# Performance work log

Measured on AMD Instinct MI355X. Metric: run time of the kernel, lower is better.

## Reference

```python
import jax, jax.numpy as jnp
import numpy as np

# Physical / solver constants (mirroring MMSolver class attrs and submodules)
GAMMA_LL = 1.7595e11   # gyromagnetic ratio (MMSolver.gamma_LL)
DT = 5e-12             # timestep [s]
ALPHA_RUN = 0.01       # Damping(relax=False)
ALPHA_RELAX = 0.5      # Damping(relax=True): high damping to relax m
A_EXCH = 3.5e-12       # exchange stiffness [J/m]
DX = 50e-9             # cell size geom.d
MU0 = 4e-7 * np.pi
C_SOT = 1e-4           # SOT strength [T]
RELAX_STEPS = 100      # MMSolver.relax_timesteps
NX, NY = 256, 256
T_STEPS = 256
N_SRC, N_PROBE, N_SIG = 3, 5, 2


def setup_inputs() -> dict:
    key = jax.random.key(0)
    list_signal = jax.random.normal(key, (N_SIG, T_STEPS, N_SRC), jnp.float32) * 1e-3
    # geometry(): constant bias field 60 mT along +y (m0 direction)
    B_ext = jnp.zeros((1, 3, NX, NY), jnp.float32).at[:, 1].set(0.06)
    Msat = jnp.float32(8e5)  # geom.Ms [A/m]
    src_pos = jnp.array([[20, 64], [20, 128], [20, 192]], jnp.int32)
    probe_pos = jnp.array([[230, 42], [230, 85], [230, 128], [230, 170], [230, 213]], jnp.int32)
    return {"list_signal": list_signal, "B_ext": B_ext, "Msat": Msat,
            "src_pos": src_pos, "probe_pos": probe_pos, "final_board": 0}


def _laplacian(m):
    # 5-point stencil with replicate (Neumann) boundaries; m: [1,3,nx,ny]
    mp = jnp.pad(m, ((0, 0), (0, 0), (1, 1), (1, 1)), mode='edge')
    return (mp[:, :, 2:, 1:-1] + mp[:, :, :-2, 1:-1]
            + mp[:, :, 1:-1, 2:] + mp[:, :, 1:-1, :-2] - 4.0 * m)


def _B_eff(m, B_ext, Msat):
    # B_ext + Exchange(m, Msat) + Demag(m, Msat)
    exch = (2.0 * A_EXCH / (Msat * DX * DX)) * _laplacian(m)
    n_demag = jnp.array([0.0, 0.0, 1.0], m.dtype).reshape(1, 3, 1, 1)  # thin-film demag
    demag = -MU0 * Msat * m * n_demag
    return B_ext + exch + demag


def _torque_LLG(m, B_ext, Msat, alpha):
    m_x_Beff = jnp.cross(m, _B_eff(m, B_ext, Msat), axis=1)
    p = jnp.broadcast_to(jnp.array([0.0, 1.0, 0.0], m.dtype).reshape(1, 3, 1, 1), m.shape)
    sot = C_SOT * jnp.cross(m, jnp.cross(m, p, axis=1), axis=1)  # torque_SOT
    return -(1.0 / (1.0 + alpha * alpha)) * (m_x_Beff + alpha * jnp.cross(m, m_x_Beff, axis=1)) + sot


def _rk4_step(m, B_ext, Msat, alpha):
    h = GAMMA_LL * DT
    k1 = _torque_LLG(m, B_ext, Msat, alpha)
    k2 = _torque_LLG(m + 0.5 * h * k1, B_ext, Msat, alpha)
    k3 = _torque_LLG(m + 0.5 * h * k2, B_ext, Msat, alpha)
    k4 = _torque_LLG(m + h * k3, B_ext, Msat, alpha)
    return m + (h / 6.0) * (k1 + 2.0 * k2 + 2.0 * k3 + k4)


def reference(list_signal, B_ext, Msat, src_pos, probe_pos, final_board):
    m0 = jnp.zeros((1, 3, NX, NY), list_signal.dtype).at[:, 1].set(1.0)

    # relax(): 100 high-damping RK4 steps under torch.no_grad()
    Bs = jax.lax.stop_gradient(B_ext)
    Ms = jax.lax.stop_gradient(Msat)
    m_relaxed, _ = jax.lax.scan(lambda m, _: (_rk4_step(m, Bs, Ms, ALPHA_RELAX), None),
                                m0, None, length=RELAX_STEPS)
    m_relaxed = jax.lax.stop_gradient(m_relaxed)

    def step(m, sig_t):
        # inject_sources: add per-source signal to B_z at source cells
        Bx = B_ext.at[0, 2, src_pos[:, 0], src_pos[:, 1]].add(sig_t)
        m_new = _rk4_step(m, Bx, Msat, ALPHA_RUN)
        # measure_probes: z-component at probe cells
        if final_board:
            meas = ((m_new - m_relaxed) * Msat)[0, 2, probe_pos[:, 0], probe_pos[:, 1]]
        else:
            meas = m_new[0, 2, probe_pos[:, 0], probe_pos[:, 1]]
        return m_new, meas

    step_ckpt = jax.checkpoint(step)  # mirrors torch.utils.checkpoint per-step
    outs = []
    for s in range(list_signal.shape[0]):  # forward()'s loop over signals
        _, probes = jax.lax.scan(step_ckpt, m_relaxed, list_signal[s])
        outs.append(probes)  # [T, n_probes]
    return jnp.stack(outs)  # [n_signals, T, n_probes]
```

## Files before the change

kernel.cpp:

```cpp
#include <hip/hip_runtime.h>

constexpr int NX = 256, NY = 256;
constexpr int T_STEPS = 256, N_SRC = 3, N_PROBE = 5;
constexpr int RELAX_STEPS = 100;
constexpr int TILE = 16, HALO = 8, LDIM = 32, LPAIR = 17;
constexpr int NBX = NX / TILE, NBY = NY / TILE;
constexpr int BPS = NBX * NBY;
constexpr int NSIG = 2;
constexpr int NBLOCKS = BPS * NSIG;
constexpr int NTHR = 512;
constexpr int NPAIR = T_STEPS / 2;
constexpr int FIELD = 3 * NX * NY;
constexpr int F_TOTAL = NSIG * 2 * FIELD;
constexpr int FLAG_STRIDE = 16;

constexpr float H_STEP = (float)(175950000000.0 * 5e-12);
constexpr float H_HALF = (float)(175950000000.0 * 5e-12 * 0.5);
constexpr float H_6    = (float)(175950000000.0 * 5e-12 / 6.0);
constexpr float CSOT   = 1e-4f;

typedef float f2 __attribute__((ext_vector_type(2)));
union F2U { f2 v; unsigned long long u; };

__global__ void init_flags(int* flags) {
    flags[blockIdx.x * blockDim.x + threadIdx.x] = 0;
}

__device__ __forceinline__ void torque2(f2 mx, f2 my, f2 mz,
                                        f2 B0, f2 B1, f2 B2,
                                        float pref, float alpha,
                                        f2& o0, f2& o1, f2& o2) {
    const f2 c10 = my * B2 - mz * B1;
    const f2 c11 = mz * B0 - mx * B2;
    const f2 c12 = mx * B1 - my * B0;
    const f2 c20 = my * c12 - mz * c11;
    const f2 c21 = mz * c10 - mx * c12;
    const f2 c22 = mx * c11 - my * c10;
    o0 = pref * (c10 + alpha * c20) + CSOT * (my * mx);
    o1 = pref * (c11 + alpha * c21) - CSOT * (mx * mx + mz * mz);
    o2 = pref * (c12 + alpha * c22) + CSOT * (my * mz);
}

__device__ __forceinline__ void relax_ode2(f2 Bx, f2 By, f2 Bz, float dmg,
                                           f2& r0, f2& r1, f2& r2) {
    r0 = 0.0f; r1 = 1.0f; r2 = 0.0f;
    const float aR = 0.5f;
    const float pR = (float)(-(1.0 / (1.0 + 0.5 * 0.5)));
    for (int it = 0; it < RELAX_STEPS; ++it) {
        f2 k10,k11,k12,k20,k21,k22,k30,k31,k32,k40,k41,k42;
        torque2(r0,r1,r2, Bx,By,Bz - dmg*r2, pR,aR, k10,k11,k12);
        f2 u0=r0+H_HALF*k10, u1=r1+H_HALF*k11, u2=r2+H_HALF*k12;
        torque2(u0,u1,u2, Bx,By,Bz - dmg*u2, pR,aR, k20,k21,k22);
        u0=r0+H_HALF*k20; u1=r1+H_HALF*k21; u2=r2+H_HALF*k22;
        torque2(u0,u1,u2, Bx,By,Bz - dmg*u2, pR,aR, k30,k31,k32);
        u0=r0+H_STEP*k30; u1=r1+H_STEP*k31; u2=r2+H_STEP*k32;
        torque2(u0,u1,u2, Bx,By,Bz - dmg*u2, pR,aR, k40,k41,k42);
        r0 += H_6 * (((k10 + 2.0f*k20) + 2.0f*k30) + k40);
        r1 += H_6 * (((k11 + 2.0f*k21) + 2.0f*k31) + k41);
        r2 += H_6 * (((k12 + 2.0f*k22) + 2.0f*k32) + k42);
    }
}

__device__ __forceinline__ float cohLoad(const float* p) {
    return __hip_atomic_load(p, __ATOMIC_RELAXED, __HIP_MEMORY_SCOPE_AGENT);
}
__device__ __forceinline__ f2 cohLoad2(const float* p) {
    F2U x; x.u = __hip_atomic_load((const unsigned long long*)p,
                                   __ATOMIC_RELAXED, __HIP_MEMORY_SCOPE_AGENT);
    return x.v;
}
__device__ __forceinline__ void cohStore2(float* p, f2 v) {
    F2U x; x.v = v;
    __hip_atomic_store((unsigned long long*)p, x.u,
                       __ATOMIC_RELAXED, __HIP_MEMORY_SCOPE_AGENT);
}

__global__ __launch_bounds__(NTHR, 4)
void mm_kernel(const float* __restrict__ sig,
               const float* __restrict__ Bext,
               const float* __restrict__ MsatP,
               const int*   __restrict__ srcp,
               const int*   __restrict__ prbp,
               const int*   __restrict__ fbP,
               float* __restrict__ out,
               float* __restrict__ F,
               int*   __restrict__ flags)
{
    __shared__ f2 bufA[3][LDIM][LPAIR];
    __shared__ f2 bufB[3][LDIM][LPAIR];

    const int tid = threadIdx.x;
    const int blk = blockIdx.x;
    const int sg = blk & 1;
    const int b  = blk >> 1;
    const int tbx = b / NBY, tby = b % NBY;
    const int x0 = tbx * TILE, y0 = tby * TILE;
    const bool atT = (tbx == 0), atB = (tbx == NBX - 1);
    const bool atL = (tby == 0), atR = (tby == NBY - 1);

    const float Msat = MsatP[0];
    const float cex = 7e-12f / (Msat * 5e-8f * 5e-8f);
    const float dmg = (float)(4e-7 * 3.14159265358979323846) * Msat;
    const int fb = fbP[0];
    const float alpha = 0.01f;
    const float pref  = (float)(-(1.0 / (1.0 + 0.01 * 0.01)));

    const int r  = tid >> 4;
    const int pp = tid & 15;
    const int c2 = pp << 1;
    const int gx  = x0 - HALO + r;
    const int gy0 = y0 - HALO + c2;
    const int gy1 = gy0 + 1;
    const int gxc  = min(max(gx, 0), NX - 1);
    const int gyc0 = min(max(gy0, 0), NY - 1);
    const int gyc1 = min(max(gy1, 0), NY - 1);
    const bool cUp = (gxc == 0), cDn = (gxc == NX - 1);
    const bool cL  = (gyc0 == 0), cR  = (gyc1 == NY - 1);
    const bool interior = (r >= HALO && r < HALO + TILE &&
                           c2 >= HALO && c2 < HALO + TILE);
    const bool pairOK = (gy0 >= 0 && gy0 <= NY - 2);
    const int srcFlagIdx = sg * BPS + (gxc >> 4) * NBY + (gyc0 >> 4);

    int sid0 = -1, sid1 = -1, pid0 = -1, pid1 = -1;
    for (int k = 0; k < N_SRC; ++k) {
        if (srcp[2*k] == gxc && srcp[2*k+1] == gyc0) sid0 = k;
        if (srcp[2*k] == gxc && srcp[2*k+1] == gyc1) sid1 = k;
    }
    if (interior)
        for (int k = 0; k < N_PROBE; ++k) {
            if (prbp[2*k] == gx && prbp[2*k+1] == gy0) pid0 = k;
            if (prbp[2*k] == gx && prbp[2*k+1] == gy1) pid1 = k;
        }

    const f2 bX = { Bext[0*NX*NY + gxc*NY + gyc0], Bext[0*NX*NY + gxc*NY + gyc1] };
    const f2 bY = { Bext[1*NX*NY + gxc*NY + gyc0], Bext[1*NX*NY + gxc*NY + gyc1] };
    const f2 bZ = { Bext[2*NX*NY + gxc*NY + gyc0], Bext[2*NX*NY + gxc*NY + gyc1] };

    f2 m0, m1, m2;
    relax_ode2(bX, bY, bZ, dmg, m0, m1, m2);
    const f2 mrelz = m2;

    f2 a0 = 0.f, a1 = 0.f, a2 = 0.f;
    f2 f0, f1, f2v;

    float* Fsig = F + (size_t)sg * 2 * FIELD;
    int* myflag = flags + (sg * BPS + b) * FLAG_STRIDE;

    bufA[0][r][pp] = m0; bufA[1][r][pp] = m1; bufA[2][r][pp] = m2;
    f0 = m0; f1 = m1; f2v = m2;

    for (int pr = 0; pr < NPAIR; ++pr) {
        if (pr > 0 && !interior) {
            const int* fp = flags + srcFlagIdx * FLAG_STRIDE;
            while (__hip_atomic_load(fp, __ATOMIC_RELAXED,
                                     __HIP_MEMORY_SCOPE_AGENT) < pr)
                __builtin_amdgcn_s_sleep(1);
            const float* Fin = Fsig + (size_t)(pr & 1) * FIELD;
            if (pairOK) {
                const int g0 = gxc * NY + gy0;
                m0 = cohLoad2(Fin + g0);
                m1 = cohLoad2(Fin + NX*NY + g0);
                m2 = cohLoad2(Fin + 2*NX*NY + g0);
            } else {
                const int gg = gxc * NY + gyc0;
                const float v0 = cohLoad(Fin + gg);
                const float v1 = cohLoad(Fin + NX*NY + gg);
                const float v2 = cohLoad(Fin + 2*NX*NY + gg);
                m0 = f2{v0, v0}; m1 = f2{v1, v1}; m2 = f2{v2, v2};
            }
            bufA[0][r][pp] = m0; bufA[1][r][pp] = m1; bufA[2][r][pp] = m2;
            f0 = m0; f1 = m1; f2v = m2;
        }
        f2 b2cs[2] = { bZ, bZ };
        if (sid0 >= 0) {
            b2cs[0].x = bZ.x + sig[((size_t)sg*T_STEPS + 2*pr    )*N_SRC + sid0];
            b2cs[1].x = bZ.x + sig[((size_t)sg*T_STEPS + 2*pr + 1)*N_SRC + sid0];
        }
        if (sid1 >= 0) {
            b2cs[0].y = bZ.y + sig[((size_t)sg*T_STEPS + 2*pr    )*N_SRC + sid1];
            b2cs[1].y = bZ.y + sig[((size_t)sg*T_STEPS + 2*pr + 1)*N_SRC + sid1];
        }
        __syncthreads();

        for (int p = 0; p < 2; ++p) {
            const f2 b2c = b2cs[p];

            for (int s = 1; s <= 4; ++s) {
                const int sh = 4*p + s;
                const int loi = atT ? HALO : sh;
                const int hiI = atB ? HALO + TILE - 1 : LDIM - 1 - sh;
                const int loj = atL ? HALO : sh;
                const int hiJ = atR ? HALO + TILE - 1 : LDIM - 1 - sh;
                const float cc = (s <= 2) ? H_HALF : H_STEP;
                const float w  = (s == 1 || s == 4) ? 1.0f : 2.0f;
                const f2 (*P)[LDIM][LPAIR] = (sh & 1) ? bufA : bufB;
                f2 (*Q)[LDIM][LPAIR] = (sh & 1) ? bufB : bufA;

                const bool active = (r >= loi && r <= hiI &&
                                     c2 + 1 >= loj && c2 <= hiJ);
                if (active) {
                    const f2 fo[3] = { f0, f1, f2v };
                    f2 l[3];
                    #pragma unroll
                    for (int ch = 0; ch < 3; ++ch) {
                        const f2 up = cUp ? fo[ch] : P[ch][r-1][pp];
                        const f2 dn = cDn ? fo[ch] : P[ch][r+1][pp];
                        const float lfs = __shfl_up(fo[ch].y, 1);
                        const float rts = __shfl_down(fo[ch].x, 1);
                        const float lf = cL ? fo[ch].x : lfs;
                        const float rt = cR ? fo[ch].y : rts;
                        const f2 rgt = { fo[ch].y, rt };
                        const f2 lft = { lf, fo[ch].x };
                        l[ch] = dn + up + rgt + lft - 4.f * fo[ch];
                    }
                    f2 t0, t1, t2;
                    torque2(f0, f1, f2v,
                            bX + cex * l[0],
                            bY + cex * l[1],
                            b2c + cex * l[2] - dmg * f2v,
                            pref, alpha, t0, t1, t2);
                    if (s < 4) {
                        const bool inr = (r >= (atT ? HALO : 4*p + 4) &&
                                          r <= (atB ? HALO+TILE-1 : 27 - 4*p) &&
                                          c2 >= (atL ? HALO : 4*p + 4) &&
                                          c2 <= (atR ? HALO+TILE-1 : 27 - 4*p));
                        if (inr) { a0 += w*t0; a1 += w*t1; a2 += w*t2; }
                        f0 = m0 + cc*t0; f1 = m1 + cc*t1; f2v = m2 + cc*t2;
                        Q[0][r][pp] = f0; Q[1][r][pp] = f1; Q[2][r][pp] = f2v;
                    } else {
                        a0 += w*t0; a1 += w*t1; a2 += w*t2;
                        m0 += H_6*a0; m1 += H_6*a1; m2 += H_6*a2;
                        a0 = 0.f; a1 = 0.f; a2 = 0.f;
                        f0 = m0; f1 = m1; f2v = m2;
                        Q[0][r][pp] = m0; Q[1][r][pp] = m1; Q[2][r][pp] = m2;
                        const int tt = 2*pr + p;
                        if (pid0 >= 0)
                            out[((size_t)sg*T_STEPS + tt)*N_PROBE + pid0] =
                                fb ? (m2.x - mrelz.x)*Msat : m2.x;
                        if (pid1 >= 0)
                            out[((size_t)sg*T_STEPS + tt)*N_PROBE + pid1] =
                                fb ? (m2.y - mrelz.y)*Msat : m2.y;
                        if (p == 1 && pr + 1 < NPAIR && interior) {
                            float* Fout = Fsig + (size_t)((pr + 1) & 1) * FIELD;
                            const int g0 = gx * NY + gy0;
                            cohStore2(Fout + g0,          m0);
                            cohStore2(Fout + NX*NY + g0,  m1);
                            cohStore2(Fout + 2*NX*NY + g0, m2);
                        }
                    }
                }
                if (p == 1 && s == 4 && pr + 1 < NPAIR)
                    __builtin_amdgcn_s_waitcnt(0);
                __syncthreads();
            }
        }
        if (pr + 1 < NPAIR && tid == 0)
            __hip_atomic_store(myflag, pr + 1, __ATOMIC_RELAXED,
                               __HIP_MEMORY_SCOPE_AGENT);
    }
}

extern "C" void kernel_launch(void* const* d_in, const int* in_sizes, int n_in,
                              void* d_out, int out_size, void* d_ws, size_t ws_size,
                              hipStream_t stream) {
    const float* sigp = (const float*)d_in[0];
    const float* Bext = (const float*)d_in[1];
    const float* Msat = (const float*)d_in[2];
    const int*   srcp = (const int*)d_in[3];
    const int*   prbp = (const int*)d_in[4];
    const int*   fbP  = (const int*)d_in[5];
    float* outp = (float*)d_out;
    float* F    = (float*)d_ws;
    int*   flags = (int*)((char*)d_ws + (size_t)F_TOTAL * sizeof(float));

    init_flags<<<NBLOCKS * FLAG_STRIDE / 256, 256, 0, stream>>>(flags);

    void* args[] = { (void*)&sigp, (void*)&Bext, (void*)&Msat, (void*)&srcp,
                     (void*)&prbp, (void*)&fbP, (void*)&outp, (void*)&F,
                     (void*)&flags };
    hipLaunchCooperativeKernel((void*)mm_kernel, dim3(NBLOCKS), dim3(NTHR),
                               args, 0, stream);
}
```

Measured before the change: 1.169 ms.

## Process both signals in one block with float4 lanes instead of separate blocks

```diff
diff --git a/kernel.cpp b/kernel.cpp
--- a/kernel.cpp
+++ b/kernel.cpp
@@ -7,7 +7,7 @@
 constexpr int NBX = NX / TILE, NBY = NY / TILE;
 constexpr int BPS = NBX * NBY;
 constexpr int NSIG = 2;
-constexpr int NBLOCKS = BPS * NSIG;
+constexpr int NBLOCKS = BPS;
 constexpr int NTHR = 512;
 constexpr int NPAIR = T_STEPS / 2;
 constexpr int FIELD = 3 * NX * NY;
@@ -20,41 +20,42 @@
 constexpr float CSOT   = 1e-4f;
 
 typedef float f2 __attribute__((ext_vector_type(2)));
+typedef float f4 __attribute__((ext_vector_type(4)));
 union F2U { f2 v; unsigned long long u; };
 
 __global__ void init_flags(int* flags) {
     flags[blockIdx.x * blockDim.x + threadIdx.x] = 0;
 }
 
-__device__ __forceinline__ void torque2(f2 mx, f2 my, f2 mz,
-                                        f2 B0, f2 B1, f2 B2,
+__device__ __forceinline__ void torque4(f4 mx, f4 my, f4 mz,
+                                        f4 B0, f4 B1, f4 B2,
                                         float pref, float alpha,
-                                        f2& o0, f2& o1, f2& o2) {
-    const f2 c10 = my * B2 - mz * B1;
-    const f2 c11 = mz * B0 - mx * B2;
-    const f2 c12 = mx * B1 - my * B0;
-    const f2 c20 = my * c12 - mz * c11;
-    const f2 c21 = mz * c10 - mx * c12;
-    const f2 c22 = mx * c11 - my * c10;
+                                        f4& o0, f4& o1, f4& o2) {
+    const f4 c10 = my * B2 - mz * B1;
+    const f4 c11 = mz * B0 - mx * B2;
+    const f4 c12 = mx * B1 - my * B0;
+    const f4 c20 = my * c12 - mz * c11;
+    const f4 c21 = mz * c10 - mx * c12;
+    const f4 c22 = mx * c11 - my * c10;
     o0 = pref * (c10 + alpha * c20) + CSOT * (my * mx);
     o1 = pref * (c11 + alpha * c21) - CSOT * (mx * mx + mz * mz);
     o2 = pref * (c12 + alpha * c22) + CSOT * (my * mz);
 }
 
-__device__ __forceinline__ void relax_ode2(f2 Bx, f2 By, f2 Bz, float dmg,
-                                           f2& r0, f2& r1, f2& r2) {
+__device__ __forceinline__ void relax_ode4(f4 Bx, f4 By, f4 Bz, float dmg,
+                                           f4& r0, f4& r1, f4& r2) {
     r0 = 0.0f; r1 = 1.0f; r2 = 0.0f;
     const float aR = 0.5f;
     const float pR = (float)(-(1.0 / (1.0 + 0.5 * 0.5)));
     for (int it = 0; it < RELAX_STEPS; ++it) {
-        f2 k10,k11,k12,k20,k21,k22,k30,k31,k32,k40,k41,k42;
-        torque2(r0,r1,r2, Bx,By,Bz - dmg*r2, pR,aR, k10,k11,k12);
-        f2 u0=r0+H_HALF*k10, u1=r1+H_HALF*k11, u2=r2+H_HALF*k12;
-        torque2(u0,u1,u2, Bx,By,Bz - dmg*u2, pR,aR, k20,k21,k22);
+        f4 k10,k11,k12,k20,k21,k22,k30,k31,k32,k40,k41,k42;
+        torque4(r0,r1,r2, Bx,By,Bz - dmg*r2, pR,aR, k10,k11,k12);
+        f4 u0=r0+H_HALF*k10, u1=r1+H_HALF*k11, u2=r2+H_HALF*k12;
+        torque4(u0,u1,u2, Bx,By,Bz - dmg*u2, pR,aR, k20,k21,k22);
         u0=r0+H_HALF*k20; u1=r1+H_HALF*k21; u2=r2+H_HALF*k22;
-        torque2(u0,u1,u2, Bx,By,Bz - dmg*u2, pR,aR, k30,k31,k32);
+        torque4(u0,u1,u2, Bx,By,Bz - dmg*u2, pR,aR, k30,k31,k32);
         u0=r0+H_STEP*k30; u1=r1+H_STEP*k31; u2=r2+H_STEP*k32;
-        torque2(u0,u1,u2, Bx,By,Bz - dmg*u2, pR,aR, k40,k41,k42);
+        torque4(u0,u1,u2, Bx,By,Bz - dmg*u2, pR,aR, k40,k41,k42);
         r0 += H_6 * (((k10 + 2.0f*k20) + 2.0f*k30) + k40);
         r1 += H_6 * (((k11 + 2.0f*k21) + 2.0f*k31) + k41);
         r2 += H_6 * (((k12 + 2.0f*k22) + 2.0f*k32) + k42);
@@ -75,7 +76,7 @@
                        __ATOMIC_RELAXED, __HIP_MEMORY_SCOPE_AGENT);
 }
 
-__global__ __launch_bounds__(NTHR, 4)
+__global__ __launch_bounds__(NTHR, 2)
 void mm_kernel(const float* __restrict__ sig,
                const float* __restrict__ Bext,
                const float* __restrict__ MsatP,
@@ -86,13 +87,11 @@
                float* __restrict__ F,
                int*   __restrict__ flags)
 {
-    __shared__ f2 bufA[3][LDIM][LPAIR];
-    __shared__ f2 bufB[3][LDIM][LPAIR];
+    __shared__ f4 bufA[3][LDIM][LPAIR];
+    __shared__ f4 bufB[3][LDIM][LPAIR];
 
     const int tid = threadIdx.x;
-    const int blk = blockIdx.x;
-    const int sg = blk & 1;
-    const int b  = blk >> 1;
+    const int b   = blockIdx.x;
     const int tbx = b / NBY, tby = b % NBY;
     const int x0 = tbx * TILE, y0 = tby * TILE;
     const bool atT = (tbx == 0), atB = (tbx == NBX - 1);
@@ -119,7 +118,7 @@
     const bool interior = (r >= HALO && r < HALO + TILE &&
                            c2 >= HALO && c2 < HALO + TILE);
     const bool pairOK = (gy0 >= 0 && gy0 <= NY - 2);
-    const int srcFlagIdx = sg * BPS + (gxc >> 4) * NBY + (gyc0 >> 4);
+    const int srcFlagIdx = (gxc >> 4) * NBY + (gyc0 >> 4);
 
     int sid0 = -1, sid1 = -1, pid0 = -1, pid1 = -1;
     for (int k = 0; k < N_SRC; ++k) {
@@ -132,19 +131,23 @@
             if (prbp[2*k] == gx && prbp[2*k+1] == gy1) pid1 = k;
         }
 
-    const f2 bX = { Bext[0*NX*NY + gxc*NY + gyc0], Bext[0*NX*NY + gxc*NY + gyc1] };
-    const f2 bY = { Bext[1*NX*NY + gxc*NY + gyc0], Bext[1*NX*NY + gxc*NY + gyc1] };
-    const f2 bZ = { Bext[2*NX*NY + gxc*NY + gyc0], Bext[2*NX*NY + gxc*NY + gyc1] };
-
-    f2 m0, m1, m2;
-    relax_ode2(bX, bY, bZ, dmg, m0, m1, m2);
-    const f2 mrelz = m2;
-
-    f2 a0 = 0.f, a1 = 0.f, a2 = 0.f;
-    f2 f0, f1, f2v;
-
-    float* Fsig = F + (size_t)sg * 2 * FIELD;
-    int* myflag = flags + (sg * BPS + b) * FLAG_STRIDE;
+    const float bx0 = Bext[0*NX*NY + gxc*NY + gyc0], bx1 = Bext[0*NX*NY + gxc*NY + gyc1];
+    const float by0 = Bext[1*NX*NY + gxc*NY + gyc0], by1 = Bext[1*NX*NY + gxc*NY + gyc1];
+    const float bz0 = Bext[2*NX*NY + gxc*NY + gyc0], bz1 = Bext[2*NX*NY + gxc*NY + gyc1];
+    const f4 bX = { bx0, bx1, bx0, bx1 };
+    const f4 bY = { by0, by1, by0, by1 };
+    const f4 bZ = { bz0, bz1, bz0, bz1 };
+
+    f4 m0, m1, m2;
+    relax_ode4(bX, bY, bZ, dmg, m0, m1, m2);
+    const f4 mrelz = m2;
+
+    f4 a0 = 0.f, a1 = 0.f, a2 = 0.f;
+    f4 f0, f1, f2v;
+
+    float* Fs0 = F;
+    float* Fs1 = F + 2 * FIELD;
+    int* myflag = flags + b * FLAG_STRIDE;
 
     bufA[0][r][pp] = m0; bufA[1][r][pp] = m1; bufA[2][r][pp] = m2;
     f0 = m0; f1 = m1; f2v = m2;
@@ -155,35 +158,43 @@
             while (__hip_atomic_load(fp, __ATOMIC_RELAXED,
                                      __HIP_MEMORY_SCOPE_AGENT) < pr)
                 __builtin_amdgcn_s_sleep(1);
-            const float* Fin = Fsig + (size_t)(pr & 1) * FIELD;
+            const float* Fin0 = Fs0 + (size_t)(pr & 1) * FIELD;
+            const float* Fin1 = Fs1 + (size_t)(pr & 1) * FIELD;
             if (pairOK) {
                 const int g0 = gxc * NY + gy0;
-                m0 = cohLoad2(Fin + g0);
-                m1 = cohLoad2(Fin + NX*NY + g0);
-                m2 = cohLoad2(Fin + 2*NX*NY + g0);
+                const f2 A0 = cohLoad2(Fin0 + g0),          B0 = cohLoad2(Fin1 + g0);
+                const f2 A1 = cohLoad2(Fin0 + NX*NY + g0),  B1 = cohLoad2(Fin1 + NX*NY + g0);
+                const f2 A2 = cohLoad2(Fin0 + 2*NX*NY + g0),B2 = cohLoad2(Fin1 + 2*NX*NY + g0);
+                m0 = f4{A0.x, A0.y, B0.x, B0.y};
+                m1 = f4{A1.x, A1.y, B1.x, B1.y};
+                m2 = f4{A2.x, A2.y, B2.x, B2.y};
             } else {
                 const int gg = gxc * NY + gyc0;
-                const float v0 = cohLoad(Fin + gg);
-                const float v1 = cohLoad(Fin + NX*NY + gg);
-                const float v2 = cohLoad(Fin + 2*NX*NY + gg);
-                m0 = f2{v0, v0}; m1 = f2{v1, v1}; m2 = f2{v2, v2};
+                const float u0 = cohLoad(Fin0 + gg),          v0 = cohLoad(Fin1 + gg);
+                const float u1 = cohLoad(Fin0 + NX*NY + gg),  v1 = cohLoad(Fin1 + NX*NY + gg);
+                const float u2 = cohLoad(Fin0 + 2*NX*NY + gg),v2 = cohLoad(Fin1 + 2*NX*NY + gg);
+                m0 = f4{u0, u0, v0, v0}; m1 = f4{u1, u1, v1, v1}; m2 = f4{u2, u2, v2, v2};
             }
             bufA[0][r][pp] = m0; bufA[1][r][pp] = m1; bufA[2][r][pp] = m2;
             f0 = m0; f1 = m1; f2v = m2;
         }
-        f2 b2cs[2] = { bZ, bZ };
-        if (sid0 >= 0) {
-            b2cs[0].x = bZ.x + sig[((size_t)sg*T_STEPS + 2*pr    )*N_SRC + sid0];
-            b2cs[1].x = bZ.x + sig[((size_t)sg*T_STEPS + 2*pr + 1)*N_SRC + sid0];
-        }
-        if (sid1 >= 0) {
-            b2cs[0].y = bZ.y + sig[((size_t)sg*T_STEPS + 2*pr    )*N_SRC + sid1];
-            b2cs[1].y = bZ.y + sig[((size_t)sg*T_STEPS + 2*pr + 1)*N_SRC + sid1];
+        f4 b2cs[2] = { bZ, bZ };
+        #pragma unroll
+        for (int p = 0; p < 2; ++p) {
+            const int tt = 2*pr + p;
+            if (sid0 >= 0) {
+                b2cs[p].x = bz0 + sig[((size_t)0*T_STEPS + tt)*N_SRC + sid0];
+                b2cs[p].z = bz0 + sig[((size_t)1*T_STEPS + tt)*N_SRC + sid0];
+            }
+            if (sid1 >= 0) {
+                b2cs[p].y = bz1 + sig[((size_t)0*T_STEPS + tt)*N_SRC + sid1];
+                b2cs[p].w = bz1 + sig[((size_t)1*T_STEPS + tt)*N_SRC + sid1];
+            }
         }
         __syncthreads();
 
         for (int p = 0; p < 2; ++p) {
-            const f2 b2c = b2cs[p];
+            const f4 b2c = b2cs[p];
 
             for (int s = 1; s <= 4; ++s) {
                 const int sh = 4*p + s;
@@ -193,28 +204,29 @@
                 const int hiJ = atR ? HALO + TILE - 1 : LDIM - 1 - sh;
                 const float cc = (s <= 2) ? H_HALF : H_STEP;
                 const float w  = (s == 1 || s == 4) ? 1.0f : 2.0f;
-                const f2 (*P)[LDIM][LPAIR] = (sh & 1) ? bufA : bufB;
-                f2 (*Q)[LDIM][LPAIR] = (sh & 1) ? bufB : bufA;
+                const f4 (*P)[LDIM][LPAIR] = (sh & 1) ? bufA : bufB;
+                f4 (*Q)[LDIM][LPAIR] = (sh & 1) ? bufB : bufA;
 
                 const bool active = (r >= loi && r <= hiI &&
                                      c2 + 1 >= loj && c2 <= hiJ);
                 if (active) {
-                    const f2 fo[3] = { f0, f1, f2v };
-                    f2 l[3];
+                    const f4 fo[3] = { f0, f1, f2v };
+                    f4 l[3];
                     #pragma unroll
                     for (int ch = 0; ch < 3; ++ch) {
-                        const f2 up = cUp ? fo[ch] : P[ch][r-1][pp];
-                        const f2 dn = cDn ? fo[ch] : P[ch][r+1][pp];
-                        const float lfs = __shfl_up(fo[ch].y, 1);
-                        const float rts = __shfl_down(fo[ch].x, 1);
-                        const float lf = cL ? fo[ch].x : lfs;
-                        const float rt = cR ? fo[ch].y : rts;
-                        const f2 rgt = { fo[ch].y, rt };
-                        const f2 lft = { lf, fo[ch].x };
+                        const f4 up = cUp ? fo[ch] : P[ch][r-1][pp];
+                        const f4 dn = cDn ? fo[ch] : P[ch][r+1][pp];
+                        float lf0, lf1, rt0, rt1;
+                        if (cL) { lf0 = fo[ch].x; lf1 = fo[ch].z; }
+                        else    { lf0 = P[ch][r][pp-1].y; lf1 = P[ch][r][pp-1].w; }
+                        if (cR) { rt0 = fo[ch].y; rt1 = fo[ch].w; }
+                        else    { rt0 = P[ch][r][pp+1].x; rt1 = P[ch][r][pp+1].z; }
+                        const f4 lft = { lf0, fo[ch].x, lf1, fo[ch].z };
+                        const f4 rgt = { fo[ch].y, rt0, fo[ch].w, rt1 };
                         l[ch] = dn + up + rgt + lft - 4.f * fo[ch];
                     }
-                    f2 t0, t1, t2;
-                    torque2(f0, f1, f2v,
+                    f4 t0, t1, t2;
+                    torque4(f0, f1, f2v,
                             bX + cex * l[0],
                             bY + cex * l[1],
                             b2c + cex * l[2] - dmg * f2v,
@@ -234,18 +246,28 @@
                         f0 = m0; f1 = m1; f2v = m2;
                         Q[0][r][pp] = m0; Q[1][r][pp] = m1; Q[2][r][pp] = m2;
                         const int tt = 2*pr + p;
-                        if (pid0 >= 0)
-                            out[((size_t)sg*T_STEPS + tt)*N_PROBE + pid0] =
+                        if (pid0 >= 0) {
+                            out[((size_t)0*T_STEPS + tt)*N_PROBE + pid0] =
                                 fb ? (m2.x - mrelz.x)*Msat : m2.x;
-                        if (pid1 >= 0)
-                            out[((size_t)sg*T_STEPS + tt)*N_PROBE + pid1] =
+                            out[((size_t)1*T_STEPS + tt)*N_PROBE + pid0] =
+                                fb ? (m2.z - mrelz.z)*Msat : m2.z;
+                        }
+                        if (pid1 >= 0) {
+                            out[((size_t)0*T_STEPS + tt)*N_PROBE + pid1] =
                                 fb ? (m2.y - mrelz.y)*Msat : m2.y;
+                            out[((size_t)1*T_STEPS + tt)*N_PROBE + pid1] =
+                                fb ? (m2.w - mrelz.w)*Msat : m2.w;
+                        }
                         if (p == 1 && pr + 1 < NPAIR && interior) {
-                            float* Fout = Fsig + (size_t)((pr + 1) & 1) * FIELD;
+                            float* Fo0 = Fs0 + (size_t)((pr + 1) & 1) * FIELD;
+                            float* Fo1 = Fs1 + (size_t)((pr + 1) & 1) * FIELD;
                             const int g0 = gx * NY + gy0;
-                            cohStore2(Fout + g0,          m0);
-                            cohStore2(Fout + NX*NY + g0,  m1);
-                            cohStore2(Fout + 2*NX*NY + g0, m2);
+                            cohStore2(Fo0 + g0,           f2{m0.x, m0.y});
+                            cohStore2(Fo1 + g0,           f2{m0.z, m0.w});
+                            cohStore2(Fo0 + NX*NY + g0,   f2{m1.x, m1.y});
+                            cohStore2(Fo1 + NX*NY + g0,   f2{m1.z, m1.w});
+                            cohStore2(Fo0 + 2*NX*NY + g0, f2{m2.x, m2.y});
+                            cohStore2(Fo1 + 2*NX*NY + g0, f2{m2.z, m2.w});
                         }
                     }
                 }
```

After: 1.338 ms. +14.5%, slower.
